# Optimization experiments

Hardware: AMD Instinct MI355X
Metric: run time of the kernel (lower is better)

## Reference

```python
import jax, jax.numpy as jnp
import numpy as np

NUM_STEPS = 5


def setup_inputs() -> dict:
    key = jax.random.key(0)
    ks = jax.random.split(key, 12)
    B, N, H, E, A = 8, 1024, 64, 2, 8
    initial_state = jax.random.normal(ks[0], (B, N, H), dtype=jnp.float32)
    annotation = jax.random.normal(ks[1], (B, N, A), dtype=jnp.float32)
    # sparse-ish positive adjacency, scaled so matmul outputs don't saturate gates
    adj_matrix = jax.random.uniform(ks[2], (B, N, 2 * N * E), dtype=jnp.float32) * 0.01
    s = 0.05
    W_edge = jax.random.normal(ks[3], (H, H * E), dtype=jnp.float32) * s
    b_edge = jax.random.normal(ks[4], (H * E,), dtype=jnp.float32) * s
    W_gate = jax.random.normal(ks[5], (3 * H, H), dtype=jnp.float32) * s
    b_gate = jax.random.normal(ks[6], (H,), dtype=jnp.float32) * s
    W_hid = jax.random.normal(ks[7], (H + A, H), dtype=jnp.float32) * s
    b_hid = jax.random.normal(ks[8], (H,), dtype=jnp.float32) * s
    W_out = jax.random.normal(ks[9], (H, 1), dtype=jnp.float32) * s
    b_out = jax.random.normal(ks[10], (1,), dtype=jnp.float32) * s
    return dict(initial_state=initial_state, annotation=annotation, adj_matrix=adj_matrix,
                W_edge=W_edge, b_edge=b_edge, W_gate=W_gate, b_gate=b_gate,
                W_hid=W_hid, b_hid=b_hid, W_out=W_out, b_out=b_out)


def reference(initial_state, annotation, adj_matrix, W_edge, b_edge,
              W_gate, b_gate, W_hid, b_hid, W_out, b_out):
    B, N, H = initial_state.shape
    E = W_edge.shape[1] // H
    boundary = N * E
    A_in = adj_matrix[:, :, :boundary]   # [B, N, N*E]
    A_out = adj_matrix[:, :, boundary:]  # [B, N, N*E]

    h = initial_state
    for _ in range(NUM_STEPS):
        # Linear(H, H*E) then view/transpose to [B, N*E, H].
        # Original computes incoming_edge and outgoing_edge with the SAME
        # linear on the SAME input -> identical tensors; compute once.
        edge = jnp.einsum('bnh,he->bne', h, W_edge) + b_edge      # [B, N, H*E]
        edge = edge.reshape(B, N, H, E).transpose(0, 3, 1, 2).reshape(B, N * E, H)
        a_in = jnp.matmul(A_in, edge)    # [B, N, H]
        a_out = jnp.matmul(A_out, edge)  # [B, N, H]
        a = jnp.concatenate([a_in, a_out, h], axis=2)             # [B, N, 3H]
        # update and reset use the same gate linear -> equal; compute once.
        z = jax.nn.sigmoid(jnp.einsum('bnk,kh->bnh', a, W_gate) + b_gate)
        a_r = jnp.concatenate([a_in, a_out, z * h], axis=2)
        h_tilde = jnp.tanh(jnp.einsum('bnk,kh->bnh', a_r, W_gate) + b_gate)
        h = (1.0 - z) * h + z * h_tilde

    # task_id not in {18, 19}: node-level output head
    ha = jnp.concatenate([h, annotation], axis=2)                 # [B, N, H+A]
    out = jnp.tanh(jnp.einsum('bnk,kh->bnh', ha, W_hid) + b_hid)  # [B, N, H]
    out = (jnp.einsum('bnh,ho->bno', out, W_out) + b_out).sum(axis=2)  # [B, N]
    return out
```

## Files before the change

kernel.cpp:

```cpp
#include <hip/hip_runtime.h>
#include <math.h>

#define BN    8
#define NN    1024
#define HH    64
#define ADIM  8
#define STEPS 5
#define K2    2048
#define ROWS  (BN*NN)

typedef __attribute__((ext_vector_type(8))) short bf16x8;
typedef __attribute__((ext_vector_type(4))) float f32x4;

__device__ __forceinline__ unsigned short f2bf(float f) {
    unsigned int u = __float_as_uint(f);
    u += 0x7FFF + ((u >> 16) & 1);
    return (unsigned short)(u >> 16);
}
__device__ __forceinline__ float bf2f(unsigned short h) {
    return __uint_as_float(((unsigned int)h) << 16);
}
__device__ __forceinline__ float ftanh(float x) {
    float e = __expf(2.f * x);
    return 1.f - 2.f / (e + 1.f);
}

__device__ __forceinline__ void lgkm_barrier() {
    asm volatile("s_waitcnt lgkmcnt(0)" ::: "memory");
    __builtin_amdgcn_s_barrier();
    asm volatile("" ::: "memory");
}


__global__ __launch_bounds__(256) void conv_adj(
    const float* __restrict__ in, unsigned short* __restrict__ out)
{
    __shared__ unsigned short tl[8][520];
    int bid = blockIdx.x;
    int kg = bid & 7;
    int ng = (bid >> 3) & 63;
    int d  = (bid >> 9) & 1;
    int b  = bid >> 10;
    int t = threadIdx.x;

    const float* src = in + ((size_t)(b * 1024 + ng * 16)) * 4096 + d * 2048 + kg * 256;
    #pragma unroll
    for (int it = 0; it < 4; ++it) {
        int u = it * 256 + t;
        int r = u >> 6, c4 = u & 63;
        float4 v = *(const float4*)(src + (size_t)r * 4096 + c4 * 4);
        int k = c4 * 4;
        int kb = k >> 5, kk = k & 31;
        ushort4 o;
        o.x = f2bf(v.x); o.y = f2bf(v.y); o.z = f2bf(v.z); o.w = f2bf(v.w);
        *(ushort4*)&tl[kb][r * 32 + kk] = o;
    }
    __syncthreads();

    unsigned short* dst = out + (((size_t)(b * 2 + d) * 64 + kg * 8) * 64 + ng) * 512;
    #pragma unroll
    for (int it = 0; it < 4; ++it) {
        int u = it * 256 + t;
        int kb = u >> 7, wo = u & 127;
        *(ushort4*)(dst + (size_t)kb * 32768 + wo * 4) = *(const ushort4*)&tl[kb][wo * 4];
    }
}

__global__ __launch_bounds__(256) void prep_pack(
    const float* __restrict__ Wg, const float* __restrict__ We,
    unsigned short* __restrict__ wgp, unsigned short* __restrict__ wep)
{
    int t = blockIdx.x * 256 + threadIdx.x;
    if (t < 12288) {
        int k = t >> 6, c = t & 63;
        float v = Wg[t];
        unsigned short hi = f2bf(v);
        unsigned short lo = f2bf(v - bf2f(hi));
        wgp[(size_t)c * 192 + k] = hi;
        wgp[(size_t)(64 + c) * 192 + k] = lo;
    } else if (t < 20480) {
        int u = t - 12288;
        int k = u >> 7, c = u & 127;
        float v = We[u];
        unsigned short hi = f2bf(v);
        unsigned short lo = f2bf(v - bf2f(hi));
        wep[(size_t)c * 64 + k] = hi;
        wep[(size_t)(128 + c) * 64 + k] = lo;
    }
}

__global__ __launch_bounds__(256) void init_kernel(
    const float* __restrict__ init_state,
    const float* __restrict__ We, const float* __restrict__ be,
    float* __restrict__ h_ws, unsigned short* __restrict__ edge_t)
{
    __shared__ float h_lds[4][65];
    int t = threadIdx.x;
    int r = t >> 6, hp = t & 63;
    int row = blockIdx.x * 4 + r;
    float hv = init_state[(size_t)row * 64 + hp];
    h_ws[(size_t)row * 64 + hp] = hv;
    h_lds[r][hp] = hv;
    __syncthreads();
    int b = row >> 10, n = row & 1023;
    #pragma unroll
    for (int e = 0; e < 2; ++e) {
        float acc = be[hp * 2 + e];
        #pragma unroll 8
        for (int c = 0; c < 64; ++c)
            acc += h_lds[r][c] * We[c * 128 + hp * 2 + e];
        edge_t[((size_t)b * 64 + hp) * K2 + e * NN + n] = f2bf(acc);
    }
}

__global__ __launch_bounds__(512) void step_kernel(
    const unsigned short* __restrict__ adjf,
    const unsigned short* __restrict__ ein,
    unsigned short* __restrict__ eout,
    float* __restrict__ h_ws,
    const unsigned short* __restrict__ wgp,
    const unsigned short* __restrict__ wep,
    const float* __restrict__ bg,
    const float* __restrict__ be,
    const float* __restrict__ ann,
    const float* __restrict__ Wh, const float* __restrict__ bh,
    const float* __restrict__ Wo, const float* __restrict__ bo,
    float* __restrict__ out,
    int mode)
{
    __shared__ __attribute__((aligned(16))) unsigned short Bs[2][64][264];
    __shared__ __attribute__((aligned(16))) unsigned short Xhi[32][200];
    __shared__ __attribute__((aligned(16))) unsigned short Xlo[32][200];
    __shared__ __attribute__((aligned(16))) float          hf [32][68];
    __shared__ __attribute__((aligned(16))) unsigned short HNhi[32][72];
    __shared__ __attribute__((aligned(16))) unsigned short HNlo[32][72];

    int t  = threadIdx.x;
    int b  = blockIdx.x >> 5;
    int mt = blockIdx.x & 31;
    int n0 = mt * 32;
    size_t hbase = ((size_t)(b * NN + n0)) * 64;

    int lane = t & 63, w = t >> 6, l15 = lane & 15, q = lane >> 4;
    int dir = w >> 2, rh = (w >> 1) & 1, kc = w & 1;
    int nb  = mt * 2 + rh;

    const unsigned short* A2 = adjf
        + (((size_t)(b * 2 + dir) * 64 + kc * 4) * 64 + nb) * 512 + l15 * 32 + q * 8;

    int srow[4], scol[4];
    const unsigned short* sptr[4];
    #pragma unroll
    for (int i = 0; i < 4; ++i) {
        int u = i * 512 + t;
        srow[i] = u >> 5; scol[i] = (u & 31) * 8;
        sptr[i] = ein + ((size_t)b * 64 + srow[i]) * K2 + scol[i];
    }

    int hr = t >> 4, hcg = (t & 15) * 4;
    float4 hv4 = *(const float4*)(h_ws + hbase + (size_t)hr * 64 + hcg);

    uint4 gA[4], gB[4];
    #pragma unroll
    for (int i = 0; i < 4; ++i) gA[i] = *(const uint4*)(sptr[i]);
    #pragma unroll
    for (int i = 0; i < 4; ++i) gB[i] = *(const uint4*)(sptr[i] + 256);
    bf16x8 afA[4], afB[4];
    #pragma unroll
    for (int ks = 0; ks < 4; ++ks)
        afA[ks] = *(const bf16x8*)(A2 + (size_t)ks * 32768);
    #pragma unroll
    for (int ks = 0; ks < 4; ++ks)
        afB[ks] = *(const bf16x8*)(A2 + (size_t)(8 + ks) * 32768);

    {
        float vv[4] = {hv4.x, hv4.y, hv4.z, hv4.w};
        #pragma unroll
        for (int j = 0; j < 4; ++j) {
            float hv = vv[j];
            unsigned short hi = f2bf(hv), lo = f2bf(hv - bf2f(hi));
            Xhi[hr][128 + hcg + j] = hi;
            Xlo[hr][128 + hcg + j] = lo;
            hf[hr][hcg + j] = hv;
        }
    }

    #pragma unroll
    for (int i = 0; i < 4; ++i)
        *(uint4*)&Bs[0][srow[i]][scol[i]] = gA[i];
    lgkm_barrier();

    f32x4 acc[4];
    #pragma unroll
    for (int ct = 0; ct < 4; ++ct) acc[ct] = (f32x4){0.f, 0.f, 0.f, 0.f};

    #pragma unroll
    for (int c = 0; c < 8; ++c) {
        const int par = c & 1;
        if (c < 6) {
            #pragma unroll
            for (int i = 0; i < 4; ++i) {
                uint4 v = *(const uint4*)(sptr[i] + (c + 2) * 256);
                if (par == 0) gA[i] = v; else gB[i] = v;
            }
        }
        #pragma unroll
        for (int ks = 0; ks < 4; ++ks) {
            bf16x8 a = (par == 0) ? afA[ks] : afB[ks];
            #pragma unroll
            for (int ct = 0; ct < 4; ++ct) {
                bf16x8 bfr = *(const bf16x8*)&Bs[par][ct * 16 + l15][kc * 128 + ks * 32 + q * 8];
                acc[ct] = __builtin_amdgcn_mfma_f32_16x16x32_bf16(a, bfr, acc[ct], 0, 0, 0);
            }
        }
        if (c < 6) {
            #pragma unroll
            for (int ks = 0; ks < 4; ++ks) {
                bf16x8 v = *(const bf16x8*)(A2 + (size_t)((c + 2) * 8 + ks) * 32768);
                if (par == 0) afA[ks] = v; else afB[ks] = v;
            }
        }
        if (c < 7) {
            #pragma unroll
            for (int i = 0; i < 4; ++i) {
                uint4 v = (par == 0) ? gB[i] : gA[i];
                *(uint4*)&Bs[par ^ 1][srow[i]][scol[i]] = v;
            }
        }
        lgkm_barrier();
    }

    float (*red)[16][68] = (float (*)[16][68])(&Bs[0][0][0]);
    int gg = w >> 1;
    if (kc == 1) {
        #pragma unroll
        for (int ct = 0; ct < 4; ++ct)
            #pragma unroll
            for (int i = 0; i < 4; ++i)
                red[gg][q * 4 + i][ct * 16 + l15] = acc[ct][i];
    }
    __syncthreads();
    if (kc == 0) {
        #pragma unroll
        for (int ct = 0; ct < 4; ++ct)
            #pragma unroll
            for (int i = 0; i < 4; ++i) {
                float v = acc[ct][i] + red[gg][q * 4 + i][ct * 16 + l15];
                unsigned short hi = f2bf(v), lo = f2bf(v - bf2f(hi));
                int r  = rh * 16 + q * 4 + i;
                int cc2 = dir * 64 + ct * 16 + l15;
                Xhi[r][cc2] = hi;
                Xlo[r][cc2] = lo;
            }
    }
    __syncthreads();

    int mg = w & 1, cg16 = w >> 1;
    int arow = mg * 16 + l15;
    int cc = cg16 * 16 + l15;
    const unsigned short* wcol = wgp + (size_t)cc * 192;
    f32x4 as = (f32x4){0.f, 0.f, 0.f, 0.f}, az;

    #pragma unroll
    for (int ks = 0; ks < 4; ++ks) {
        bf16x8 ah = *(const bf16x8*)&Xhi[arow][ks * 32 + q * 8];
        bf16x8 al = *(const bf16x8*)&Xlo[arow][ks * 32 + q * 8];
        const unsigned short* wb = wcol + ks * 32 + q * 8;
        bf16x8 bh2 = *(const bf16x8*)wb;
        bf16x8 bl2 = *(const bf16x8*)(wb + 64 * 192);
        as = __builtin_amdgcn_mfma_f32_16x16x32_bf16(ah, bh2, as, 0, 0, 0);
        as = __builtin_amdgcn_mfma_f32_16x16x32_bf16(ah, bl2, as, 0, 0, 0);
        as = __builtin_amdgcn_mfma_f32_16x16x32_bf16(al, bh2, as, 0, 0, 0);
    }
    az = as;
    #pragma unroll
    for (int ks = 4; ks < 6; ++ks) {
        bf16x8 ah = *(const bf16x8*)&Xhi[arow][ks * 32 + q * 8];
        bf16x8 al = *(const bf16x8*)&Xlo[arow][ks * 32 + q * 8];
        const unsigned short* wb = wcol + ks * 32 + q * 8;
        bf16x8 bh2 = *(const bf16x8*)wb;
        bf16x8 bl2 = *(const bf16x8*)(wb + 64 * 192);
        az = __builtin_amdgcn_mfma_f32_16x16x32_bf16(ah, bh2, az, 0, 0, 0);
        az = __builtin_amdgcn_mfma_f32_16x16x32_bf16(ah, bl2, az, 0, 0, 0);
        az = __builtin_amdgcn_mfma_f32_16x16x32_bf16(al, bh2, az, 0, 0, 0);
    }
    __syncthreads();

    float zv[4], hv[4];
    float bgv = bg[cc];
    #pragma unroll
    for (int i = 0; i < 4; ++i) {
        int r = mg * 16 + q * 4 + i;
        float z = 1.f / (1.f + __expf(-(az[i] + bgv)));
        float h = hf[r][cc];
        zv[i] = z; hv[i] = h;
        float zh = z * h;
        unsigned short hi = f2bf(zh), lo = f2bf(zh - bf2f(hi));
        Xhi[r][128 + cc] = hi;
        Xlo[r][128 + cc] = lo;
    }
    __syncthreads();

    #pragma unroll
    for (int ks = 4; ks < 6; ++ks) {
        bf16x8 ah = *(const bf16x8*)&Xhi[arow][ks * 32 + q * 8];
        bf16x8 al = *(const bf16x8*)&Xlo[arow][ks * 32 + q * 8];
        const unsigned short* wb = wcol + ks * 32 + q * 8;
        bf16x8 bh2 = *(const bf16x8*)wb;
        bf16x8 bl2 = *(const bf16x8*)(wb + 64 * 192);
        as = __builtin_amdgcn_mfma_f32_16x16x32_bf16(ah, bh2, as, 0, 0, 0);
        as = __builtin_amdgcn_mfma_f32_16x16x32_bf16(ah, bl2, as, 0, 0, 0);
        as = __builtin_amdgcn_mfma_f32_16x16x32_bf16(al, bh2, as, 0, 0, 0);
    }

    #pragma unroll
    for (int i = 0; i < 4; ++i) {
        int r = mg * 16 + q * 4 + i;
        float ht = ftanh(as[i] + bgv);
        float z  = zv[i];
        float hn = (1.f - z) * hv[i] + z * ht;
        if (mode == 0) {
            h_ws[hbase + (size_t)r * 64 + cc] = hn;
            unsigned short hi = f2bf(hn), lo = f2bf(hn - bf2f(hi));
            HNhi[r][cc] = hi;
            HNlo[r][cc] = lo;
        } else {
            hf[r][cc] = hn;
        }
    }
    __syncthreads();

    if (mode == 0) {
        int me = w & 1, cb2 = (w >> 1) * 2;
        int erow = me * 16 + l15;
        f32x4 ae[2];
        ae[0] = ae[1] = (f32x4){0.f, 0.f, 0.f, 0.f};
        #pragma unroll
        for (int ks = 0; ks < 2; ++ks) {
            bf16x8 ah = *(const bf16x8*)&HNhi[erow][ks * 32 + q * 8];
            bf16x8 al = *(const bf16x8*)&HNlo[erow][ks * 32 + q * 8];
            #pragma unroll
            for (int p = 0; p < 2; ++p) {
                int ec = (cb2 + p) * 16 + l15;
                const unsigned short* wb = wep + (size_t)ec * 64 + ks * 32 + q * 8;
                bf16x8 bh2 = *(const bf16x8*)wb;
                bf16x8 bl2 = *(const bf16x8*)(wb + 128 * 64);
                ae[p] = __builtin_amdgcn_mfma_f32_16x16x32_bf16(ah, bh2, ae[p], 0, 0, 0);
                ae[p] = __builtin_amdgcn_mfma_f32_16x16x32_bf16(ah, bl2, ae[p], 0, 0, 0);
                ae[p] = __builtin_amdgcn_mfma_f32_16x16x32_bf16(al, bh2, ae[p], 0, 0, 0);
            }
        }
        #pragma unroll
        for (int p = 0; p < 2; ++p) {
            int ec = (cb2 + p) * 16 + l15;
            float bev = be[ec];
            int hp2 = ec >> 1, e = ec & 1;
            size_t ebase = ((size_t)b * 64 + hp2) * K2 + (size_t)e * NN
                         + n0 + me * 16 + q * 4;
            ushort4 ev;
            ev.x = f2bf(ae[p][0] + bev);
            ev.y = f2bf(ae[p][1] + bev);
            ev.z = f2bf(ae[p][2] + bev);
            ev.w = f2bf(ae[p][3] + bev);
            *(ushort4*)(eout + ebase) = ev;
        }
    } else {
        int r = t >> 4, hq = (t & 15) * 4;
        int row = b * NN + n0 + r;
        float av[ADIM];
        #pragma unroll
        for (int j = 0; j < ADIM; ++j) av[j] = ann[(size_t)row * ADIM + j];
        float ac2[4];
        #pragma unroll
        for (int i = 0; i < 4; ++i) ac2[i] = bh[hq + i];
        #pragma unroll 8
        for (int k = 0; k < 64; ++k) {
            float hv2 = hf[r][k];
            float4 wv = *(const float4*)&Wh[k * 64 + hq];
            ac2[0] += hv2 * wv.x; ac2[1] += hv2 * wv.y;
            ac2[2] += hv2 * wv.z; ac2[3] += hv2 * wv.w;
        }
        #pragma unroll
        for (int k = 0; k < ADIM; ++k) {
            float4 wv = *(const float4*)&Wh[(64 + k) * 64 + hq];
            ac2[0] += av[k] * wv.x; ac2[1] += av[k] * wv.y;
            ac2[2] += av[k] * wv.z; ac2[3] += av[k] * wv.w;
        }
        float v = 0.f;
        #pragma unroll
        for (int i = 0; i < 4; ++i)
            v += ftanh(ac2[i]) * Wo[hq + i];
        #pragma unroll
        for (int m = 8; m; m >>= 1) v += __shfl_xor(v, m, 64);
        if ((t & 15) == 0) out[row] = v + bo[0];
    }
}

extern "C" void kernel_launch(void* const* d_in, const int* in_sizes, int n_in,
                              void* d_out, int out_size, void* d_ws, size_t ws_size,
                              hipStream_t stream) {
    const float* init_state = (const float*)d_in[0];
    const float* ann = (const float*)d_in[1];
    const float* adj = (const float*)d_in[2];
    const float* We  = (const float*)d_in[3];
    const float* be  = (const float*)d_in[4];
    const float* Wg  = (const float*)d_in[5];
    const float* bg  = (const float*)d_in[6];
    const float* Wh  = (const float*)d_in[7];
    const float* bh  = (const float*)d_in[8];
    const float* Wo  = (const float*)d_in[9];
    const float* bo  = (const float*)d_in[10];
    float* out = (float*)d_out;

    char* wsb = (char*)d_ws;
    unsigned short* adjf   = (unsigned short*)wsb;
    unsigned short* edge_a = (unsigned short*)(wsb + 67108864);
    unsigned short* edge_b = (unsigned short*)(wsb + 69206016);
    float*          h_ws   = (float*)(wsb + 71303168);
    unsigned short* wgp    = (unsigned short*)(wsb + 73400320);
    unsigned short* wep    = (unsigned short*)(wsb + 73449472);

    conv_adj<<<dim3(8192), dim3(256), 0, stream>>>(adj, adjf);
    prep_pack<<<dim3(80), dim3(256), 0, stream>>>(Wg, We, wgp, wep);
    init_kernel<<<dim3(ROWS / 4), dim3(256), 0, stream>>>(init_state, We, be, h_ws, edge_a);
    for (int s = 0; s < STEPS; ++s) {
        const unsigned short* ein = (s & 1) ? edge_b : edge_a;
        unsigned short* eo        = (s & 1) ? edge_a : edge_b;
        step_kernel<<<dim3(256), dim3(512), 0, stream>>>(
            adjf, ein, eo, h_ws, wgp, wep, bg, be,
            ann, Wh, bh, Wo, bo, out, (s == STEPS - 1) ? 1 : 0);
    }
}
```

Before: 377.4 us.

## Fuse GGNN steps into persistent cooperative kernel with register-resident adjacency

Replaces the five per-step kernel launches with one cooperative persistent kernel that loops over steps and uses grid.sync between them. Each block's slice of the bf16 adjacency is loaded once into 32 vector registers and reused across all steps, and the hidden state stays in shared memory, so the global h workspace is removed. This cuts repeated adjacency reads, launch gaps and h round-trips. In exchange it adds grid-wide barriers and heavy register pressure from the register-held adjacency, which could cause spills.

```diff
diff --git a/kernel.cpp b/kernel.cpp
--- a/kernel.cpp
+++ b/kernel.cpp
@@ -1,5 +1,8 @@
 #include <hip/hip_runtime.h>
+#include <hip/hip_cooperative_groups.h>
 #include <math.h>
+
+namespace cg = cooperative_groups;
 
 #define BN    8
 #define NN    1024
@@ -92,14 +95,13 @@
 __global__ __launch_bounds__(256) void init_kernel(
     const float* __restrict__ init_state,
     const float* __restrict__ We, const float* __restrict__ be,
-    float* __restrict__ h_ws, unsigned short* __restrict__ edge_t)
+    unsigned short* __restrict__ edge_t)
 {
     __shared__ float h_lds[4][65];
     int t = threadIdx.x;
     int r = t >> 6, hp = t & 63;
     int row = blockIdx.x * 4 + r;
     float hv = init_state[(size_t)row * 64 + hp];
-    h_ws[(size_t)row * 64 + hp] = hv;
     h_lds[r][hp] = hv;
     __syncthreads();
     int b = row >> 10, n = row & 1023;
@@ -113,20 +115,19 @@
     }
 }
 
-__global__ __launch_bounds__(512) void step_kernel(
+__global__ __launch_bounds__(512, 2) void persist(
+    const float* __restrict__ init_state,
+    const float* __restrict__ ann,
     const unsigned short* __restrict__ adjf,
-    const unsigned short* __restrict__ ein,
-    unsigned short* __restrict__ eout,
-    float* __restrict__ h_ws,
+    unsigned short* __restrict__ edge_a,
+    unsigned short* __restrict__ edge_b,
     const unsigned short* __restrict__ wgp,
     const unsigned short* __restrict__ wep,
     const float* __restrict__ bg,
     const float* __restrict__ be,
-    const float* __restrict__ ann,
     const float* __restrict__ Wh, const float* __restrict__ bh,
     const float* __restrict__ Wo, const float* __restrict__ bo,
-    float* __restrict__ out,
-    int mode)
+    float* __restrict__ out)
 {
     __shared__ __attribute__((aligned(16))) unsigned short Bs[2][64][264];
     __shared__ __attribute__((aligned(16))) unsigned short Xhi[32][200];
@@ -135,6 +136,8 @@
     __shared__ __attribute__((aligned(16))) unsigned short HNhi[32][72];
     __shared__ __attribute__((aligned(16))) unsigned short HNlo[32][72];
 
+    cg::grid_group grid = cg::this_grid();
+
     int t  = threadIdx.x;
     int b  = blockIdx.x >> 5;
     int mt = blockIdx.x & 31;
@@ -145,226 +148,219 @@
     int dir = w >> 2, rh = (w >> 1) & 1, kc = w & 1;
     int nb  = mt * 2 + rh;
 
+    int hr = t >> 4, hcg = (t & 15) * 4;
+    {
+        float4 v = *(const float4*)(init_state + hbase + (size_t)hr * 64 + hcg);
+        hf[hr][hcg + 0] = v.x; hf[hr][hcg + 1] = v.y;
+        hf[hr][hcg + 2] = v.z; hf[hr][hcg + 3] = v.w;
+    }
+
     const unsigned short* A2 = adjf
         + (((size_t)(b * 2 + dir) * 64 + kc * 4) * 64 + nb) * 512 + l15 * 32 + q * 8;
+    bf16x8 areg[32];
+    #pragma unroll
+    for (int c = 0; c < 8; ++c)
+        #pragma unroll
+        for (int ks = 0; ks < 4; ++ks)
+            areg[c * 4 + ks] = *(const bf16x8*)(A2 + (size_t)(c * 8 + ks) * 32768);
 
     int srow[4], scol[4];
-    const unsigned short* sptr[4];
+    size_t boff[4];
     #pragma unroll
     for (int i = 0; i < 4; ++i) {
         int u = i * 512 + t;
         srow[i] = u >> 5; scol[i] = (u & 31) * 8;
-        sptr[i] = ein + ((size_t)b * 64 + srow[i]) * K2 + scol[i];
-    }
-
-    int hr = t >> 4, hcg = (t & 15) * 4;
-    float4 hv4 = *(const float4*)(h_ws + hbase + (size_t)hr * 64 + hcg);
-
-    uint4 gA[4], gB[4];
-    #pragma unroll
-    for (int i = 0; i < 4; ++i) gA[i] = *(const uint4*)(sptr[i]);
-    #pragma unroll
-    for (int i = 0; i < 4; ++i) gB[i] = *(const uint4*)(sptr[i] + 256);
-    bf16x8 afA[4], afB[4];
-    #pragma unroll
-    for (int ks = 0; ks < 4; ++ks)
-        afA[ks] = *(const bf16x8*)(A2 + (size_t)ks * 32768);
-    #pragma unroll
-    for (int ks = 0; ks < 4; ++ks)
-        afB[ks] = *(const bf16x8*)(A2 + (size_t)(8 + ks) * 32768);
-
-    {
-        float vv[4] = {hv4.x, hv4.y, hv4.z, hv4.w};
-        #pragma unroll
-        for (int j = 0; j < 4; ++j) {
-            float hv = vv[j];
-            unsigned short hi = f2bf(hv), lo = f2bf(hv - bf2f(hi));
-            Xhi[hr][128 + hcg + j] = hi;
-            Xlo[hr][128 + hcg + j] = lo;
-            hf[hr][hcg + j] = hv;
-        }
-    }
-
-    #pragma unroll
-    for (int i = 0; i < 4; ++i)
-        *(uint4*)&Bs[0][srow[i]][scol[i]] = gA[i];
-    lgkm_barrier();
-
-    f32x4 acc[4];
-    #pragma unroll
-    for (int ct = 0; ct < 4; ++ct) acc[ct] = (f32x4){0.f, 0.f, 0.f, 0.f};
-
-    #pragma unroll
-    for (int c = 0; c < 8; ++c) {
-        const int par = c & 1;
-        if (c < 6) {
-            #pragma unroll
-            for (int i = 0; i < 4; ++i) {
-                uint4 v = *(const uint4*)(sptr[i] + (c + 2) * 256);
-                if (par == 0) gA[i] = v; else gB[i] = v;
-            }
-        }
-        #pragma unroll
-        for (int ks = 0; ks < 4; ++ks) {
-            bf16x8 a = (par == 0) ? afA[ks] : afB[ks];
-            #pragma unroll
-            for (int ct = 0; ct < 4; ++ct) {
-                bf16x8 bfr = *(const bf16x8*)&Bs[par][ct * 16 + l15][kc * 128 + ks * 32 + q * 8];
-                acc[ct] = __builtin_amdgcn_mfma_f32_16x16x32_bf16(a, bfr, acc[ct], 0, 0, 0);
-            }
-        }
-        if (c < 6) {
-            #pragma unroll
-            for (int ks = 0; ks < 4; ++ks) {
-                bf16x8 v = *(const bf16x8*)(A2 + (size_t)((c + 2) * 8 + ks) * 32768);
-                if (par == 0) afA[ks] = v; else afB[ks] = v;
-            }
-        }
-        if (c < 7) {
-            #pragma unroll
-            for (int i = 0; i < 4; ++i) {
-                uint4 v = (par == 0) ? gB[i] : gA[i];
-                *(uint4*)&Bs[par ^ 1][srow[i]][scol[i]] = v;
-            }
-        }
-        lgkm_barrier();
-    }
-
-    float (*red)[16][68] = (float (*)[16][68])(&Bs[0][0][0]);
-    int gg = w >> 1;
-    if (kc == 1) {
-        #pragma unroll
-        for (int ct = 0; ct < 4; ++ct)
-            #pragma unroll
-            for (int i = 0; i < 4; ++i)
-                red[gg][q * 4 + i][ct * 16 + l15] = acc[ct][i];
-    }
-    __syncthreads();
-    if (kc == 0) {
-        #pragma unroll
-        for (int ct = 0; ct < 4; ++ct)
-            #pragma unroll
-            for (int i = 0; i < 4; ++i) {
-                float v = acc[ct][i] + red[gg][q * 4 + i][ct * 16 + l15];
-                unsigned short hi = f2bf(v), lo = f2bf(v - bf2f(hi));
-                int r  = rh * 16 + q * 4 + i;
-                int cc2 = dir * 64 + ct * 16 + l15;
-                Xhi[r][cc2] = hi;
-                Xlo[r][cc2] = lo;
-            }
-    }
-    __syncthreads();
+        boff[i] = ((size_t)b * 64 + srow[i]) * K2 + scol[i];
+    }
 
     int mg = w & 1, cg16 = w >> 1;
     int arow = mg * 16 + l15;
     int cc = cg16 * 16 + l15;
     const unsigned short* wcol = wgp + (size_t)cc * 192;
-    f32x4 as = (f32x4){0.f, 0.f, 0.f, 0.f}, az;
-
-    #pragma unroll
-    for (int ks = 0; ks < 4; ++ks) {
-        bf16x8 ah = *(const bf16x8*)&Xhi[arow][ks * 32 + q * 8];
-        bf16x8 al = *(const bf16x8*)&Xlo[arow][ks * 32 + q * 8];
-        const unsigned short* wb = wcol + ks * 32 + q * 8;
-        bf16x8 bh2 = *(const bf16x8*)wb;
-        bf16x8 bl2 = *(const bf16x8*)(wb + 64 * 192);
-        as = __builtin_amdgcn_mfma_f32_16x16x32_bf16(ah, bh2, as, 0, 0, 0);
-        as = __builtin_amdgcn_mfma_f32_16x16x32_bf16(ah, bl2, as, 0, 0, 0);
-        as = __builtin_amdgcn_mfma_f32_16x16x32_bf16(al, bh2, as, 0, 0, 0);
-    }
-    az = as;
-    #pragma unroll
-    for (int ks = 4; ks < 6; ++ks) {
-        bf16x8 ah = *(const bf16x8*)&Xhi[arow][ks * 32 + q * 8];
-        bf16x8 al = *(const bf16x8*)&Xlo[arow][ks * 32 + q * 8];
-        const unsigned short* wb = wcol + ks * 32 + q * 8;
-        bf16x8 bh2 = *(const bf16x8*)wb;
-        bf16x8 bl2 = *(const bf16x8*)(wb + 64 * 192);
-        az = __builtin_amdgcn_mfma_f32_16x16x32_bf16(ah, bh2, az, 0, 0, 0);
-        az = __builtin_amdgcn_mfma_f32_16x16x32_bf16(ah, bl2, az, 0, 0, 0);
-        az = __builtin_amdgcn_mfma_f32_16x16x32_bf16(al, bh2, az, 0, 0, 0);
-    }
+    float bgv = bg[cc];
+
     __syncthreads();
 
-    float zv[4], hv[4];
-    float bgv = bg[cc];
-    #pragma unroll
-    for (int i = 0; i < 4; ++i) {
-        int r = mg * 16 + q * 4 + i;
-        float z = 1.f / (1.f + __expf(-(az[i] + bgv)));
-        float h = hf[r][cc];
-        zv[i] = z; hv[i] = h;
-        float zh = z * h;
-        unsigned short hi = f2bf(zh), lo = f2bf(zh - bf2f(hi));
-        Xhi[r][128 + cc] = hi;
-        Xlo[r][128 + cc] = lo;
-    }
-    __syncthreads();
-
-    #pragma unroll
-    for (int ks = 4; ks < 6; ++ks) {
-        bf16x8 ah = *(const bf16x8*)&Xhi[arow][ks * 32 + q * 8];
-        bf16x8 al = *(const bf16x8*)&Xlo[arow][ks * 32 + q * 8];
-        const unsigned short* wb = wcol + ks * 32 + q * 8;
-        bf16x8 bh2 = *(const bf16x8*)wb;
-        bf16x8 bl2 = *(const bf16x8*)(wb + 64 * 192);
-        as = __builtin_amdgcn_mfma_f32_16x16x32_bf16(ah, bh2, as, 0, 0, 0);
-        as = __builtin_amdgcn_mfma_f32_16x16x32_bf16(ah, bl2, as, 0, 0, 0);
-        as = __builtin_amdgcn_mfma_f32_16x16x32_bf16(al, bh2, as, 0, 0, 0);
-    }
-
-    #pragma unroll
-    for (int i = 0; i < 4; ++i) {
-        int r = mg * 16 + q * 4 + i;
-        float ht = ftanh(as[i] + bgv);
-        float z  = zv[i];
-        float hn = (1.f - z) * hv[i] + z * ht;
-        if (mode == 0) {
-            h_ws[hbase + (size_t)r * 64 + cc] = hn;
-            unsigned short hi = f2bf(hn), lo = f2bf(hn - bf2f(hi));
-            HNhi[r][cc] = hi;
-            HNlo[r][cc] = lo;
-        } else {
+    for (int s = 0; s < STEPS; ++s) {
+        const unsigned short* eb = (s & 1) ? edge_b : edge_a;
+        unsigned short* eo       = (s & 1) ? edge_a : edge_b;
+
+        #pragma unroll
+        for (int j = 0; j < 4; ++j) {
+            float hv = hf[hr][hcg + j];
+            unsigned short hi = f2bf(hv), lo = f2bf(hv - bf2f(hi));
+            Xhi[hr][128 + hcg + j] = hi;
+            Xlo[hr][128 + hcg + j] = lo;
+        }
+
+        uint4 g[4];
+        #pragma unroll
+        for (int i = 0; i < 4; ++i) g[i] = *(const uint4*)(eb + boff[i]);
+        #pragma unroll
+        for (int i = 0; i < 4; ++i) *(uint4*)&Bs[0][srow[i]][scol[i]] = g[i];
+        lgkm_barrier();
+
+        f32x4 acc[4];
+        #pragma unroll
+        for (int ct = 0; ct < 4; ++ct) acc[ct] = (f32x4){0.f, 0.f, 0.f, 0.f};
+
+        #pragma unroll
+        for (int c = 0; c < 8; ++c) {
+            const int par = c & 1;
+            if (c < 7) {
+                #pragma unroll
+                for (int i = 0; i < 4; ++i)
+                    g[i] = *(const uint4*)(eb + boff[i] + (c + 1) * 256);
+            }
+            #pragma unroll
+            for (int ks = 0; ks < 4; ++ks) {
+                bf16x8 a = areg[c * 4 + ks];
+                #pragma unroll
+                for (int ct = 0; ct < 4; ++ct) {
+                    bf16x8 bfr = *(const bf16x8*)&Bs[par][ct * 16 + l15][kc * 128 + ks * 32 + q * 8];
+                    acc[ct] = __builtin_amdgcn_mfma_f32_16x16x32_bf16(a, bfr, acc[ct], 0, 0, 0);
+                }
+            }
+            if (c < 7) {
+                #pragma unroll
+                for (int i = 0; i < 4; ++i)
+                    *(uint4*)&Bs[par ^ 1][srow[i]][scol[i]] = g[i];
+            }
+            lgkm_barrier();
+        }
+
+        float (*red)[16][68] = (float (*)[16][68])(&Bs[0][0][0]);
+        int gg = w >> 1;
+        if (kc == 1) {
+            #pragma unroll
+            for (int ct = 0; ct < 4; ++ct)
+                #pragma unroll
+                for (int i = 0; i < 4; ++i)
+                    red[gg][q * 4 + i][ct * 16 + l15] = acc[ct][i];
+        }
+        __syncthreads();
+        if (kc == 0) {
+            #pragma unroll
+            for (int ct = 0; ct < 4; ++ct)
+                #pragma unroll
+                for (int i = 0; i < 4; ++i) {
+                    float v = acc[ct][i] + red[gg][q * 4 + i][ct * 16 + l15];
+                    unsigned short hi = f2bf(v), lo = f2bf(v - bf2f(hi));
+                    int r  = rh * 16 + q * 4 + i;
+                    int cc2 = dir * 64 + ct * 16 + l15;
+                    Xhi[r][cc2] = hi;
+                    Xlo[r][cc2] = lo;
+                }
+        }
+        __syncthreads();
+
+        f32x4 as = (f32x4){0.f, 0.f, 0.f, 0.f}, az;
+        #pragma unroll
+        for (int ks = 0; ks < 4; ++ks) {
+            bf16x8 ah = *(const bf16x8*)&Xhi[arow][ks * 32 + q * 8];
+            bf16x8 al = *(const bf16x8*)&Xlo[arow][ks * 32 + q * 8];
+            const unsigned short* wb = wcol + ks * 32 + q * 8;
+            bf16x8 bh2 = *(const bf16x8*)wb;
+            bf16x8 bl2 = *(const bf16x8*)(wb + 64 * 192);
+            as = __builtin_amdgcn_mfma_f32_16x16x32_bf16(ah, bh2, as, 0, 0, 0);
+            as = __builtin_amdgcn_mfma_f32_16x16x32_bf16(ah, bl2, as, 0, 0, 0);
+            as = __builtin_amdgcn_mfma_f32_16x16x32_bf16(al, bh2, as, 0, 0, 0);
+        }
+        az = as;
+        #pragma unroll
+        for (int ks = 4; ks < 6; ++ks) {
+            bf16x8 ah = *(const bf16x8*)&Xhi[arow][ks * 32 + q * 8];
+            bf16x8 al = *(const bf16x8*)&Xlo[arow][ks * 32 + q * 8];
+            const unsigned short* wb = wcol + ks * 32 + q * 8;
+            bf16x8 bh2 = *(const bf16x8*)wb;
+            bf16x8 bl2 = *(const bf16x8*)(wb + 64 * 192);
+            az = __builtin_amdgcn_mfma_f32_16x16x32_bf16(ah, bh2, az, 0, 0, 0);
+            az = __builtin_amdgcn_mfma_f32_16x16x32_bf16(ah, bl2, az, 0, 0, 0);
+            az = __builtin_amdgcn_mfma_f32_16x16x32_bf16(al, bh2, az, 0, 0, 0);
+        }
+        __syncthreads();
+
+        float zv[4], hv[4];
+        #pragma unroll
+        for (int i = 0; i < 4; ++i) {
+            int r = mg * 16 + q * 4 + i;
+            float z = 1.f / (1.f + __expf(-(az[i] + bgv)));
+            float h = hf[r][cc];
+            zv[i] = z; hv[i] = h;
+            float zh = z * h;
+            unsigned short hi = f2bf(zh), lo = f2bf(zh - bf2f(hi));
+            Xhi[r][128 + cc] = hi;
+            Xlo[r][128 + cc] = lo;
+        }
+        __syncthreads();
+
+        #pragma unroll
+        for (int ks = 4; ks < 6; ++ks) {
+            bf16x8 ah = *(const bf16x8*)&Xhi[arow][ks * 32 + q * 8];
+            bf16x8 al = *(const bf16x8*)&Xlo[arow][ks * 32 + q * 8];
+            const unsigned short* wb = wcol + ks * 32 + q * 8;
+            bf16x8 bh2 = *(const bf16x8*)wb;
+            bf16x8 bl2 = *(const bf16x8*)(wb + 64 * 192);
+            as = __builtin_amdgcn_mfma_f32_16x16x32_bf16(ah, bh2, as, 0, 0, 0);
+            as = __builtin_amdgcn_mfma_f32_16x16x32_bf16(ah, bl2, as, 0, 0, 0);
+            as = __builtin_amdgcn_mfma_f32_16x16x32_bf16(al, bh2, as, 0, 0, 0);
+        }
+
+        #pragma unroll
+        for (int i = 0; i < 4; ++i) {
+            int r = mg * 16 + q * 4 + i;
+            float ht = ftanh(as[i] + bgv);
+            float z  = zv[i];
+            float hn = (1.f - z) * hv[i] + z * ht;
             hf[r][cc] = hn;
-        }
-    }
-    __syncthreads();
-
-    if (mode == 0) {
-        int me = w & 1, cb2 = (w >> 1) * 2;
-        int erow = me * 16 + l15;
-        f32x4 ae[2];
-        ae[0] = ae[1] = (f32x4){0.f, 0.f, 0.f, 0.f};
-        #pragma unroll
-        for (int ks = 0; ks < 2; ++ks) {
-            bf16x8 ah = *(const bf16x8*)&HNhi[erow][ks * 32 + q * 8];
-            bf16x8 al = *(const bf16x8*)&HNlo[erow][ks * 32 + q * 8];
+            if (s < STEPS - 1) {
+                unsigned short hi = f2bf(hn), lo = f2bf(hn - bf2f(hi));
+                HNhi[r][cc] = hi;
+                HNlo[r][cc] = lo;
+            }
+        }
+        __syncthreads();
+
+        if (s < STEPS - 1) {
+            int me = w & 1, cb2 = (w >> 1) * 2;
+            int erow = me * 16 + l15;
+            f32x4 ae[2];
+            ae[0] = ae[1] = (f32x4){0.f, 0.f, 0.f, 0.f};
+            #pragma unroll
+            for (int ks = 0; ks < 2; ++ks) {
+                bf16x8 ah = *(const bf16x8*)&HNhi[erow][ks * 32 + q * 8];
+                bf16x8 al = *(const bf16x8*)&HNlo[erow][ks * 32 + q * 8];
+                #pragma unroll
+                for (int p = 0; p < 2; ++p) {
+                    int ec = (cb2 + p) * 16 + l15;
+                    const unsigned short* wb = wep + (size_t)ec * 64 + ks * 32 + q * 8;
+                    bf16x8 bh2 = *(const bf16x8*)wb;
+                    bf16x8 bl2 = *(const bf16x8*)(wb + 128 * 64);
+                    ae[p] = __builtin_amdgcn_mfma_f32_16x16x32_bf16(ah, bh2, ae[p], 0, 0, 0);
+                    ae[p] = __builtin_amdgcn_mfma_f32_16x16x32_bf16(ah, bl2, ae[p], 0, 0, 0);
+                    ae[p] = __builtin_amdgcn_mfma_f32_16x16x32_bf16(al, bh2, ae[p], 0, 0, 0);
+                }
+            }
             #pragma unroll
             for (int p = 0; p < 2; ++p) {
                 int ec = (cb2 + p) * 16 + l15;
-                const unsigned short* wb = wep + (size_t)ec * 64 + ks * 32 + q * 8;
-                bf16x8 bh2 = *(const bf16x8*)wb;
-                bf16x8 bl2 = *(const bf16x8*)(wb + 128 * 64);
-                ae[p] = __builtin_amdgcn_mfma_f32_16x16x32_bf16(ah, bh2, ae[p], 0, 0, 0);
-                ae[p] = __builtin_amdgcn_mfma_f32_16x16x32_bf16(ah, bl2, ae[p], 0, 0, 0);
-                ae[p] = __builtin_amdgcn_mfma_f32_16x16x32_bf16(al, bh2, ae[p], 0, 0, 0);
-            }
-        }
-        #pragma unroll
-        for (int p = 0; p < 2; ++p) {
-            int ec = (cb2 + p) * 16 + l15;
-            float bev = be[ec];
-            int hp2 = ec >> 1, e = ec & 1;
-            size_t ebase = ((size_t)b * 64 + hp2) * K2 + (size_t)e * NN
-                         + n0 + me * 16 + q * 4;
-            ushort4 ev;
-            ev.x = f2bf(ae[p][0] + bev);
-            ev.y = f2bf(ae[p][1] + bev);
-            ev.z = f2bf(ae[p][2] + bev);
-            ev.w = f2bf(ae[p][3] + bev);
-            *(ushort4*)(eout + ebase) = ev;
-        }
-    } else {
+                float bev = be[ec];
+                int hp2 = ec >> 1, e = ec & 1;
+                size_t ebase = ((size_t)b * 64 + hp2) * K2 + (size_t)e * NN
+                             + n0 + me * 16 + q * 4;
+                ushort4 ev;
+                ev.x = f2bf(ae[p][0] + bev);
+                ev.y = f2bf(ae[p][1] + bev);
+                ev.z = f2bf(ae[p][2] + bev);
+                ev.w = f2bf(ae[p][3] + bev);
+                *(ushort4*)(eo + ebase) = ev;
+            }
+            __threadfence();
+            grid.sync();
+        }
+    }
+
+    {
         int r = t >> 4, hq = (t & 15) * 4;
         int row = b * NN + n0 + r;
         float av[ADIM];
@@ -416,18 +412,19 @@
     unsigned short* adjf   = (unsigned short*)wsb;
     unsigned short* edge_a = (unsigned short*)(wsb + 67108864);
     unsigned short* edge_b = (unsigned short*)(wsb + 69206016);
-    float*          h_ws   = (float*)(wsb + 71303168);
-    unsigned short* wgp    = (unsigned short*)(wsb + 73400320);
-    unsigned short* wep    = (unsigned short*)(wsb + 73449472);
+    unsigned short* wgp    = (unsigned short*)(wsb + 71303168);
+    unsigned short* wep    = (unsigned short*)(wsb + 71352320);
 
     conv_adj<<<dim3(8192), dim3(256), 0, stream>>>(adj, adjf);
     prep_pack<<<dim3(80), dim3(256), 0, stream>>>(Wg, We, wgp, wep);
-    init_kernel<<<dim3(ROWS / 4), dim3(256), 0, stream>>>(init_state, We, be, h_ws, edge_a);
-    for (int s = 0; s < STEPS; ++s) {
-        const unsigned short* ein = (s & 1) ? edge_b : edge_a;
-        unsigned short* eo        = (s & 1) ? edge_a : edge_b;
-        step_kernel<<<dim3(256), dim3(512), 0, stream>>>(
-            adjf, ein, eo, h_ws, wgp, wep, bg, be,
-            ann, Wh, bh, Wo, bo, out, (s == STEPS - 1) ? 1 : 0);
-    }
-}
+    init_kernel<<<dim3(ROWS / 4), dim3(256), 0, stream>>>(init_state, We, be, edge_a);
+
+    void* args[] = {
+        (void*)&init_state, (void*)&ann, (void*)&adjf,
+        (void*)&edge_a, (void*)&edge_b, (void*)&wgp, (void*)&wep,
+        (void*)&bg, (void*)&be, (void*)&Wh, (void*)&bh,
+        (void*)&Wo, (void*)&bo, (void*)&out
+    };
+    hipLaunchCooperativeKernel((const void*)persist, dim3(256), dim3(512),
+                               args, 0, stream);
+}
```

New measurement: 759.9 us. 2.01x slower.

## Stream edge tiles directly into LDS with triple-buffered async global loads

Applied to the files above, without the earlier changes.

Replaces the register-staged double buffer for the edge (B operand) tiles with global_load_lds direct-to-LDS transfers into a triple buffer, using an XOR swizzle instead of row padding to avoid bank conflicts. Loads for chunk c+3 are issued after each compute phase, and hand-tuned vmcnt waits plus barriers order them. The aim is to free registers and remove the VGPR-to-LDS copy instructions so more of the load latency is hidden. In exchange the kernel relies on fragile manual vmcnt counting that interleaves with the A-fragment global loads, and adds an extra barrier per iteration.

```diff
diff --git a/kernel.cpp b/kernel.cpp
--- a/kernel.cpp
+++ b/kernel.cpp
@@ -12,6 +12,13 @@
 typedef __attribute__((ext_vector_type(8))) short bf16x8;
 typedef __attribute__((ext_vector_type(4))) float f32x4;
 
+typedef __attribute__((address_space(3))) unsigned int as3_uint;
+typedef __attribute__((address_space(1))) const unsigned int as1_uint;
+
+__device__ __forceinline__ void gload_lds16(const void* g, void* l) {
+    __builtin_amdgcn_global_load_lds((as1_uint*)g, (as3_uint*)l, 16, 0, 0);
+}
+
 __device__ __forceinline__ unsigned short f2bf(float f) {
     unsigned int u = __float_as_uint(f);
     u += 0x7FFF + ((u >> 16) & 1);
@@ -23,12 +30,6 @@
 __device__ __forceinline__ float ftanh(float x) {
     float e = __expf(2.f * x);
     return 1.f - 2.f / (e + 1.f);
-}
-
-__device__ __forceinline__ void lgkm_barrier() {
-    asm volatile("s_waitcnt lgkmcnt(0)" ::: "memory");
-    __builtin_amdgcn_s_barrier();
-    asm volatile("" ::: "memory");
 }
 
 
@@ -128,7 +129,7 @@
     float* __restrict__ out,
     int mode)
 {
-    __shared__ __attribute__((aligned(16))) unsigned short Bs[2][64][264];
+    __shared__ __attribute__((aligned(16))) unsigned short Bst[3][64][256];
     __shared__ __attribute__((aligned(16))) unsigned short Xhi[32][200];
     __shared__ __attribute__((aligned(16))) unsigned short Xlo[32][200];
     __shared__ __attribute__((aligned(16))) float          hf [32][68];
@@ -148,23 +149,21 @@
     const unsigned short* A2 = adjf
         + (((size_t)(b * 2 + dir) * 64 + kc * 4) * 64 + nb) * 512 + l15 * 32 + q * 8;
 
-    int srow[4], scol[4];
-    const unsigned short* sptr[4];
-    #pragma unroll
-    for (int i = 0; i < 4; ++i) {
-        int u = i * 512 + t;
-        srow[i] = u >> 5; scol[i] = (u & 31) * 8;
-        sptr[i] = ein + ((size_t)b * 64 + srow[i]) * K2 + scol[i];
-    }
-
     int hr = t >> 4, hcg = (t & 15) * 4;
     float4 hv4 = *(const float4*)(h_ws + hbase + (size_t)hr * 64 + hcg);
 
-    uint4 gA[4], gB[4];
-    #pragma unroll
-    for (int i = 0; i < 4; ++i) gA[i] = *(const uint4*)(sptr[i]);
-    #pragma unroll
-    for (int i = 0; i < 4; ++i) gB[i] = *(const uint4*)(sptr[i] + 256);
+    int lhalf = lane >> 5;
+    const char* gbase[4];
+    #pragma unroll
+    for (int i = 0; i < 4; ++i) {
+        int row = w * 8 + i * 2 + lhalf;
+        int swz = ((lane & 31) * 16) ^ (((i * 2 + lhalf) & 7) << 4);
+        gbase[i] = (const char*)ein + (size_t)(b * 64 + row) * 4096 + swz;
+    }
+    char* BstB = (char*)&Bst[0][0][0];
+    unsigned int ldsoff = (unsigned int)(w * 4096);
+
+    asm volatile("" ::: "memory");
     bf16x8 afA[4], afB[4];
     #pragma unroll
     for (int ks = 0; ks < 4; ++ks)
@@ -172,6 +171,13 @@
     #pragma unroll
     for (int ks = 0; ks < 4; ++ks)
         afB[ks] = *(const bf16x8*)(A2 + (size_t)(8 + ks) * 32768);
+    asm volatile("" ::: "memory");
+    #pragma unroll
+    for (int c = 0; c < 3; ++c)
+        #pragma unroll
+        for (int i = 0; i < 4; ++i)
+            gload_lds16(gbase[i] + c * 512, BstB + c * 32768 + ldsoff + i * 1024);
+    asm volatile("" ::: "memory");
 
     {
         float vv[4] = {hv4.x, hv4.y, hv4.z, hv4.w};
@@ -185,34 +191,37 @@
         }
     }
 
-    #pragma unroll
-    for (int i = 0; i < 4; ++i)
-        *(uint4*)&Bs[0][srow[i]][scol[i]] = gA[i];
-    lgkm_barrier();
-
     f32x4 acc[4];
     #pragma unroll
     for (int ct = 0; ct < 4; ++ct) acc[ct] = (f32x4){0.f, 0.f, 0.f, 0.f};
 
+    int swcol[4];
+    #pragma unroll
+    for (int ks = 0; ks < 4; ++ks)
+        swcol[ks] = (kc * 256 + ks * 64 + q * 16) ^ ((l15 & 7) << 4);
+
     #pragma unroll
     for (int c = 0; c < 8; ++c) {
+        const int buf = c % 3;
         const int par = c & 1;
-        if (c < 6) {
-            #pragma unroll
-            for (int i = 0; i < 4; ++i) {
-                uint4 v = *(const uint4*)(sptr[i] + (c + 2) * 256);
-                if (par == 0) gA[i] = v; else gB[i] = v;
-            }
-        }
+        if      (c == 0) asm volatile("s_waitcnt vmcnt(8)"  ::: "memory");
+        else if (c <  6) asm volatile("s_waitcnt vmcnt(12)" ::: "memory");
+        else if (c == 6) asm volatile("s_waitcnt vmcnt(8)"  ::: "memory");
+        else             asm volatile("s_waitcnt vmcnt(0)"  ::: "memory");
+        __builtin_amdgcn_s_barrier();
+
         #pragma unroll
         for (int ks = 0; ks < 4; ++ks) {
             bf16x8 a = (par == 0) ? afA[ks] : afB[ks];
             #pragma unroll
             for (int ct = 0; ct < 4; ++ct) {
-                bf16x8 bfr = *(const bf16x8*)&Bs[par][ct * 16 + l15][kc * 128 + ks * 32 + q * 8];
+                bf16x8 bfr = *(const bf16x8*)(BstB + buf * 32768
+                              + (ct * 16 + l15) * 512 + swcol[ks]);
                 acc[ct] = __builtin_amdgcn_mfma_f32_16x16x32_bf16(a, bfr, acc[ct], 0, 0, 0);
             }
         }
+        __builtin_amdgcn_s_barrier();
+        asm volatile("" ::: "memory");
         if (c < 6) {
             #pragma unroll
             for (int ks = 0; ks < 4; ++ks) {
@@ -220,17 +229,16 @@
                 if (par == 0) afA[ks] = v; else afB[ks] = v;
             }
         }
-        if (c < 7) {
-            #pragma unroll
-            for (int i = 0; i < 4; ++i) {
-                uint4 v = (par == 0) ? gB[i] : gA[i];
-                *(uint4*)&Bs[par ^ 1][srow[i]][scol[i]] = v;
-            }
-        }
-        lgkm_barrier();
-    }
-
-    float (*red)[16][68] = (float (*)[16][68])(&Bs[0][0][0]);
+        asm volatile("" ::: "memory");
+        if (c < 5) {
+            #pragma unroll
+            for (int i = 0; i < 4; ++i)
+                gload_lds16(gbase[i] + (c + 3) * 512, BstB + buf * 32768 + ldsoff + i * 1024);
+        }
+        asm volatile("" ::: "memory");
+    }
+
+    float (*red)[16][68] = (float (*)[16][68])(BstB);
     int gg = w >> 1;
     if (kc == 1) {
         #pragma unroll
```

Result: slower. 388.5 us (+2.9%).
